# Performance work log

Hardware: AMD Instinct MI355X
Metric: run time of the kernel (lower is better)

The kernel has to match this reference:

```python
import jax, jax.numpy as jnp
import numpy as np

TEMPERATURE = 0.5
EPS = 1e-8


def setup_inputs() -> dict:
    key = jax.random.key(0)
    k1, k2 = jax.random.split(key)
    B, D = 4096, 128
    z_i = jax.random.normal(k1, (B, D), dtype=jnp.float32)
    z_j = jax.random.normal(k2, (B, D), dtype=jnp.float32)
    return {"z_i": z_i, "z_j": z_j}


def reference(z_i, z_j):
    B = z_i.shape[0]
    N = 2 * B
    z = jnp.concatenate([z_i, z_j], axis=0)  # [N, D]
    # cosine similarity == normalize then Gram matrix (torch clamps denom by eps)
    norm = jnp.maximum(jnp.linalg.norm(z, axis=1, keepdims=True), EPS)
    zn = z / norm
    sim = (zn @ zn.T) / TEMPERATURE  # [N, N]
    # positive pairs sit on the +B / -B diagonals
    pos = jnp.concatenate([jnp.diagonal(sim, B), jnp.diagonal(sim, -B)])  # [N]
    # CE with label 0 over [pos | negatives(mask)] == logsumexp over all
    # non-self-diagonal entries minus the positive logit (pos re-enters the
    # logit row exactly once, so the union is: full row minus self-diagonal).
    neg_inf = jnp.asarray(-jnp.inf, dtype=sim.dtype)
    idx = jnp.arange(N)
    sim_masked = jnp.where(idx[:, None] == idx[None, :], neg_inf, sim)
    row_loss = jax.nn.logsumexp(sim_masked, axis=1) - pos  # [N]
    loss = jnp.sum(row_loss) / N  # CrossEntropyLoss(reduction='sum') / N
    return loss
```

## Files before the change

kernel.cpp:

```cpp
#include <hip/hip_runtime.h>
#include <hip/hip_bf16.h>

typedef __attribute__((ext_vector_type(8))) short short8;
typedef __attribute__((ext_vector_type(4))) float f32x4;
typedef __attribute__((address_space(1))) const unsigned int glb_u32;
typedef __attribute__((address_space(3))) unsigned int lds_u32;

#define DIMD 128
#define NSPLIT 16
#define WR 64
#define ROWS_PER_BLOCK 256
#define CPS 64

#define ZSCALE 1.69864363f
#define LN2 0.6931471805599453f

__global__ __launch_bounds__(256) void nrm_kernel(const float* __restrict__ zi,
                                                  const float* __restrict__ zj,
                                                  __hip_bfloat16* __restrict__ zn,
                                                  float* __restrict__ out, int B) {
  if (blockIdx.x == 0 && threadIdx.x == 0) out[0] = 0.0f;
  int wave = threadIdx.x >> 6, lane = threadIdx.x & 63;
  int N = 2 * B;
  int row = blockIdx.x * 4 + wave;
  if (row >= N) return;
  const float* src = (row < B) ? (zi + (size_t)row * DIMD)
                               : (zj + (size_t)(row - B) * DIMD);
  float2 v = *(const float2*)(src + lane * 2);
  float ss = v.x * v.x + v.y * v.y;
  #pragma unroll
  for (int off = 32; off; off >>= 1) ss += __shfl_xor(ss, off);
  float nrm = sqrtf(ss);
  float r = ZSCALE / fmaxf(nrm, 1e-8f);
  __hip_bfloat16* dst = zn + (size_t)row * DIMD + lane * 2;
  dst[0] = __float2bfloat16(v.x * r);
  dst[1] = __float2bfloat16(v.y * r);
}


#define STAGE(BUF, ST)                                                        \
  {                                                                           \
    const ushort* s_ = gsrc0 + (size_t)(ST) * (CPS * DIMD);                   \
    _Pragma("unroll")                                                         \
    for (int c_ = 0; c_ < 4; ++c_)                                            \
      __builtin_amdgcn_global_load_lds(                                       \
          (glb_u32*)(s_ + c_ * 16 * DIMD),                                    \
          (lds_u32*)&lds[BUF][(c_ * 16 + wave * 4) * DIMD], 16, 0, 0);        \
  }

#define COMPUTE(BUF, CC)                                                      \
  {                                                                           \
    _Pragma("unroll")                                                         \
    for (int sub = 0; sub < 4; ++sub) {                                       \
      const ushort* lp_ = &lds[BUF][(sub * 16 + l15) * DIMD];                 \
      short8 bb[4];                                                           \
      _Pragma("unroll")                                                       \
      for (int kc = 0; kc < 4; ++kc)                                          \
        bb[kc] = *(const short8*)(lp_ + roff[kc]);                            \
      const int gt_ = ((CC) >> 4) + sub;                                      \
      _Pragma("unroll")                                                       \
      for (int rg = 0; rg < 4; ++rg) {                                        \
        f32x4 acc = {0.f, 0.f, 0.f, 0.f};                                     \
        acc = __builtin_amdgcn_mfma_f32_16x16x32_bf16(a[rg][0], bb[0], acc, 0, 0, 0); \
        acc = __builtin_amdgcn_mfma_f32_16x16x32_bf16(a[rg][1], bb[1], acc, 0, 0, 0); \
        acc = __builtin_amdgcn_mfma_f32_16x16x32_bf16(a[rg][2], bb[2], acc, 0, 0, 0); \
        acc = __builtin_amdgcn_mfma_f32_16x16x32_bf16(a[rg][3], bb[3], acc, 0, 0, 0); \
        if (gt_ == diagT[rg] || gt_ == partT[rg]) {                           \
          _Pragma("unroll")                                                   \
          for (int r = 0; r < 4; ++r) {                                       \
            int i_ = R + rg * 16 + lh * 4 + r;    \
            int jg_ = (CC) + sub * 16 + l15;      \
            if (jg_ == ((i_ + B) & (N - 1))) pos[i_] = acc[r] * LN2;          \
            if (jg_ != i_) rs[rg][r] += __builtin_amdgcn_exp2f(acc[r]);       \
          }                                                                   \
        } else {                                                              \
          _Pragma("unroll")                                                   \
          for (int r = 0; r < 4; ++r)                                         \
            rs[rg][r] += __builtin_amdgcn_exp2f(acc[r]);                      \
        }                                                                     \
      }                                                                       \
    }                                                                         \
  }

__global__ __launch_bounds__(256) void sim_kernel(const __hip_bfloat16* __restrict__ znb,
                                                  float* __restrict__ partial,
                                                  float* __restrict__ pos, int B) {
  const ushort* zn = (const ushort*)znb;
  const int N = 2 * B;
  const int tid = threadIdx.x;
  const int wave = tid >> 6, lane = tid & 63;
  const int l15 = lane & 15, lh = lane >> 4;
  const int R = blockIdx.x * ROWS_PER_BLOCK + wave * WR;
  const int colsPerSplit = N / NSPLIT;
  const int C0 = blockIdx.y * colsPerSplit;
  const int NST = colsPerSplit / CPS;

  __shared__ ushort lds[2][CPS * DIMD];

  const int myCol = wave * 4 + lh;
  const int myKb = l15 ^ (myCol & 7);
  const ushort* gsrc0 = zn + (size_t)(C0 + myCol) * DIMD + myKb * 8;

  STAGE(0, 0);

  short8 a[4][4];
  #pragma unroll
  for (int rg = 0; rg < 4; ++rg) {
    const ushort* ar = zn + (size_t)(R + rg * 16 + l15) * DIMD + lh * 8;
    #pragma unroll
    for (int kc = 0; kc < 4; ++kc) a[rg][kc] = *(const short8*)(ar + kc * 32);
  }

  float rs[4][4];
  #pragma unroll
  for (int rg = 0; rg < 4; ++rg)
    #pragma unroll
    for (int r = 0; r < 4; ++r) rs[rg][r] = 0.0f;

  int diagT[4], partT[4];
  #pragma unroll
  for (int rg = 0; rg < 4; ++rg) {
    diagT[rg] = (R + rg * 16) >> 4;
    partT[rg] = ((R + rg * 16 + B) & (N - 1)) >> 4;
  }

  int roff[4];
  #pragma unroll
  for (int kc = 0; kc < 4; ++kc) roff[kc] = ((kc * 4 + lh) ^ (l15 & 7)) * 8;

  for (int st = 0; st < NST; ++st) {
    __syncthreads();
    if (st + 1 < NST) STAGE((st + 1) & 1, st + 1);
    COMPUTE(st & 1, C0 + st * CPS);
  }

  #pragma unroll
  for (int rg = 0; rg < 4; ++rg) {
    #pragma unroll
    for (int r = 0; r < 4; ++r) {
      #pragma unroll
      for (int off = 1; off < 16; off <<= 1)
        rs[rg][r] += __shfl_xor(rs[rg][r], off);
    }
  }
  if (l15 == 0) {
    #pragma unroll
    for (int rg = 0; rg < 4; ++rg)
      #pragma unroll
      for (int r = 0; r < 4; ++r)
        partial[(size_t)(R + rg * 16 + lh * 4 + r) * NSPLIT + blockIdx.y] = rs[rg][r];
  }
}

__global__ __launch_bounds__(256) void fin_kernel(const float* __restrict__ partial,
                                                  const float* __restrict__ pos,
                                                  float* __restrict__ out, int N) {
  int i = blockIdx.x * 256 + threadIdx.x;
  float li = 0.0f;
  if (i < N) {
    float s = 0.0f;
    #pragma unroll
    for (int q = 0; q < NSPLIT; ++q) s += partial[(size_t)i * NSPLIT + q];
    li = __builtin_amdgcn_logf(s) * LN2 - pos[i];
  }
  #pragma unroll
  for (int off = 32; off; off >>= 1) li += __shfl_xor(li, off);
  __shared__ float red[4];
  int wave = threadIdx.x >> 6, lane = threadIdx.x & 63;
  if (lane == 0) red[wave] = li;
  __syncthreads();
  if (threadIdx.x == 0) {
    float bs = red[0] + red[1] + red[2] + red[3];
    atomicAdd(out, bs / (float)N);
  }
}

extern "C" void kernel_launch(void* const* d_in, const int* in_sizes, int n_in,
                              void* d_out, int out_size, void* d_ws, size_t ws_size,
                              hipStream_t stream) {
  const float* zi = (const float*)d_in[0];
  const float* zj = (const float*)d_in[1];
  const int B = in_sizes[0] / DIMD;
  const int N = 2 * B;
  float* out = (float*)d_out;

  char* ws = (char*)d_ws;
  __hip_bfloat16* zn = (__hip_bfloat16*)ws;
  float* partial = (float*)(ws + (size_t)N * DIMD * 2);
  float* pos = (float*)(ws + (size_t)N * DIMD * 2 + (size_t)N * NSPLIT * 4);

  nrm_kernel<<<N / 4, 256, 0, stream>>>(zi, zj, zn, out, B);
  dim3 g2(N / ROWS_PER_BLOCK, NSPLIT);
  sim_kernel<<<g2, 256, 0, stream>>>(zn, partial, pos, B);
  fin_kernel<<<N / 256, 256, 0, stream>>>(partial, pos, out, N);
}
```

Baseline: 39.15 us.

## Double-buffer LDS B-fragment loads, raise column splits and set occupancy hint

Splits the per-stage compute into explicit LDS fragment loads and MFMA sub-steps, using two register buffers so the next sub-tile's LDS reads are issued before the current sub-tile's MFMAs and exp work. This is meant to hide LDS read latency behind matrix math. It also doubles the column split count, giving twice as many blocks with half the stages each to improve CU fill, and adds a launch-bounds occupancy hint of 4 blocks. The costs are more partial sums for the finalize kernel to reduce, shorter per-block pipelines, and possible register pressure from the extra fragment buffers under the occupancy cap.

```diff
diff --git a/kernel.cpp b/kernel.cpp
--- a/kernel.cpp
+++ b/kernel.cpp
@@ -7,7 +7,7 @@
 typedef __attribute__((address_space(3))) unsigned int lds_u32;
 
 #define DIMD 128
-#define NSPLIT 16
+#define NSPLIT 32
 #define WR 64
 #define ROWS_PER_BLOCK 256
 #define CPS 64
@@ -48,43 +48,42 @@
           (lds_u32*)&lds[BUF][(c_ * 16 + wave * 4) * DIMD], 16, 0, 0);        \
   }
 
-#define COMPUTE(BUF, CC)                                                      \
+#define LDB(BB, BUF, SUB)                                                     \
   {                                                                           \
+    const ushort* lp_ = &lds[BUF][((SUB) * 16 + l15) * DIMD];                 \
     _Pragma("unroll")                                                         \
-    for (int sub = 0; sub < 4; ++sub) {                                       \
-      const ushort* lp_ = &lds[BUF][(sub * 16 + l15) * DIMD];                 \
-      short8 bb[4];                                                           \
-      _Pragma("unroll")                                                       \
-      for (int kc = 0; kc < 4; ++kc)                                          \
-        bb[kc] = *(const short8*)(lp_ + roff[kc]);                            \
-      const int gt_ = ((CC) >> 4) + sub;                                      \
-      _Pragma("unroll")                                                       \
-      for (int rg = 0; rg < 4; ++rg) {                                        \
-        f32x4 acc = {0.f, 0.f, 0.f, 0.f};                                     \
-        acc = __builtin_amdgcn_mfma_f32_16x16x32_bf16(a[rg][0], bb[0], acc, 0, 0, 0); \
-        acc = __builtin_amdgcn_mfma_f32_16x16x32_bf16(a[rg][1], bb[1], acc, 0, 0, 0); \
-        acc = __builtin_amdgcn_mfma_f32_16x16x32_bf16(a[rg][2], bb[2], acc, 0, 0, 0); \
-        acc = __builtin_amdgcn_mfma_f32_16x16x32_bf16(a[rg][3], bb[3], acc, 0, 0, 0); \
-        if (gt_ == diagT[rg] || gt_ == partT[rg]) {                           \
-          _Pragma("unroll")                                                   \
-          for (int r = 0; r < 4; ++r) {                                       \
-            int i_ = R + rg * 16 + lh * 4 + r;    \
-            int jg_ = (CC) + sub * 16 + l15;      \
-            if (jg_ == ((i_ + B) & (N - 1))) pos[i_] = acc[r] * LN2;          \
-            if (jg_ != i_) rs[rg][r] += __builtin_amdgcn_exp2f(acc[r]);       \
-          }                                                                   \
-        } else {                                                              \
-          _Pragma("unroll")                                                   \
-          for (int r = 0; r < 4; ++r)                                         \
-            rs[rg][r] += __builtin_amdgcn_exp2f(acc[r]);                      \
+    for (int kc = 0; kc < 4; ++kc) BB[kc] = *(const short8*)(lp_ + roff[kc]); \
+  }
+
+#define MMA_SUB(BB, CC, SUB)                                                  \
+  {                                                                           \
+    const int gt_ = ((CC) >> 4) + (SUB);                                      \
+    _Pragma("unroll")                                                         \
+    for (int rg = 0; rg < 4; ++rg) {                                          \
+      f32x4 acc = {0.f, 0.f, 0.f, 0.f};                                       \
+      acc = __builtin_amdgcn_mfma_f32_16x16x32_bf16(a[rg][0], BB[0], acc, 0, 0, 0); \
+      acc = __builtin_amdgcn_mfma_f32_16x16x32_bf16(a[rg][1], BB[1], acc, 0, 0, 0); \
+      acc = __builtin_amdgcn_mfma_f32_16x16x32_bf16(a[rg][2], BB[2], acc, 0, 0, 0); \
+      acc = __builtin_amdgcn_mfma_f32_16x16x32_bf16(a[rg][3], BB[3], acc, 0, 0, 0); \
+      if (gt_ == diagT[rg] || gt_ == partT[rg]) {                             \
+        _Pragma("unroll")                                                     \
+        for (int r = 0; r < 4; ++r) {                                         \
+          int i_ = R + rg * 16 + lh * 4 + r;      \
+          int jg_ = (CC) + (SUB) * 16 + l15;      \
+          if (jg_ == ((i_ + B) & (N - 1))) pos[i_] = acc[r] * LN2;            \
+          if (jg_ != i_) rs[rg][r] += __builtin_amdgcn_exp2f(acc[r]);         \
         }                                                                     \
+      } else {                                                                \
+        _Pragma("unroll")                                                     \
+        for (int r = 0; r < 4; ++r)                                           \
+          rs[rg][r] += __builtin_amdgcn_exp2f(acc[r]);                        \
       }                                                                       \
     }                                                                         \
   }
 
-__global__ __launch_bounds__(256) void sim_kernel(const __hip_bfloat16* __restrict__ znb,
-                                                  float* __restrict__ partial,
-                                                  float* __restrict__ pos, int B) {
+__global__ __launch_bounds__(256, 4) void sim_kernel(const __hip_bfloat16* __restrict__ znb,
+                                                     float* __restrict__ partial,
+                                                     float* __restrict__ pos, int B) {
   const ushort* zn = (const ushort*)znb;
   const int N = 2 * B;
   const int tid = threadIdx.x;
@@ -128,10 +127,20 @@
   #pragma unroll
   for (int kc = 0; kc < 4; ++kc) roff[kc] = ((kc * 4 + lh) ^ (l15 & 7)) * 8;
 
+  short8 bbA[4], bbB[4];
   for (int st = 0; st < NST; ++st) {
+    const int C = C0 + st * CPS;
+    const int buf = st & 1;
     __syncthreads();
-    if (st + 1 < NST) STAGE((st + 1) & 1, st + 1);
-    COMPUTE(st & 1, C0 + st * CPS);
+    if (st + 1 < NST) STAGE(buf ^ 1, st + 1);
+    LDB(bbA, buf, 0);
+    LDB(bbB, buf, 1);
+    MMA_SUB(bbA, C, 0);
+    LDB(bbA, buf, 2);
+    MMA_SUB(bbB, C, 1);
+    LDB(bbB, buf, 3);
+    MMA_SUB(bbA, C, 2);
+    MMA_SUB(bbB, C, 3);
   }
 
   #pragma unroll
```

Result: slower. 73.84 us (+88.6%).
